# Kernel tuning notes

Measured on AMD Instinct MI355X. Metric: run time of the kernel, lower is better.

Reference implementation:

```python
import jax, jax.numpy as jnp
import numpy as np

B, N, K = 4, 2048, 48
NUM_RBF = 16
NUM_PE = 16
MAX_REL = 32
EDGE_C = 128
PE_IN = 2 * MAX_REL + 2  # 66


def setup_inputs() -> dict:
    key = jax.random.key(0)
    ks = jax.random.split(key, 10)
    coords = jax.random.normal(ks[0], (B, N, 3), dtype=jnp.float32) * 10.0
    token_exists_mask = jnp.ones((B, N), dtype=jnp.float32)
    token_bonds = (jax.random.uniform(ks[1], (B, N, N)) < 0.01).astype(jnp.float32)
    pe_w = jax.random.normal(ks[2], (PE_IN, NUM_PE), dtype=jnp.float32) * 0.05
    pe_b = jnp.zeros((NUM_PE,), dtype=jnp.float32)
    edge_w = jax.random.normal(ks[3], (NUM_PE + NUM_RBF + 1, EDGE_C), dtype=jnp.float32) * 0.05
    ln_g = jnp.ones((EDGE_C,), dtype=jnp.float32)
    ln_b = jnp.zeros((EDGE_C,), dtype=jnp.float32)
    token_to_center_atom = jax.random.randint(ks[4], (B, N), 0, N, dtype=jnp.int32)
    residue_index = jnp.sort(jax.random.randint(ks[5], (B, N), 0, 4096, dtype=jnp.int32), axis=-1)
    asym_id = jax.random.randint(ks[6], (B, N), 0, 4, dtype=jnp.int32)
    is_ligand = jax.random.randint(ks[7], (B, N), 0, 2, dtype=jnp.int32)
    return {
        'coords': coords, 'token_exists_mask': token_exists_mask,
        'token_bonds': token_bonds, 'pe_w': pe_w, 'pe_b': pe_b,
        'edge_w': edge_w, 'ln_g': ln_g, 'ln_b': ln_b,
        'token_to_center_atom': token_to_center_atom,
        'residue_index': residue_index, 'asym_id': asym_id,
        'is_ligand': is_ligand,
    }


def _gather_edges(M, E_idx):
    # M: [B, N, N], E_idx: [B, N, K] -> [B, N, K]
    return jnp.take_along_axis(M, E_idx, axis=2)


def _rbf(D):
    # D: [..., K] -> [..., K, NUM_RBF]
    D_mu = jnp.linspace(2.0, 22.0, NUM_RBF)
    D_sigma = (22.0 - 2.0) / NUM_RBF
    return jnp.exp(-(((D[..., None] - D_mu) / D_sigma) ** 2))


def reference(coords, token_exists_mask, token_bonds, pe_w, pe_b, edge_w,
              ln_g, ln_b, token_to_center_atom, residue_index, asym_id, is_ligand):
    # token coords: center atom per token, masked
    X = jnp.take_along_axis(coords, token_to_center_atom[..., None], axis=1)
    X = X * token_exists_mask[..., None]  # [B, N, 3]

    # masked pairwise distances + KNN (smallest K, sorted ascending)
    mask = token_exists_mask
    mask_2d = mask[:, None, :] * mask[:, :, None]  # [B, N, N]
    dX = X[:, :, None, :] - X[:, None, :, :]
    D = mask_2d * jnp.sqrt(jnp.sum(dX * dX, axis=-1) + 1e-6)
    D_max = jnp.max(D, axis=-1, keepdims=True)
    D_adjust = D + (1.0 - mask_2d) * D_max
    neg_D, E_idx = jax.lax.top_k(-D_adjust, K)  # largest of -D == smallest of D
    D_neighbors = -neg_D  # [B, N, K]

    RBF_all = _rbf(D_neighbors)  # [B, N, K, NUM_RBF]

    # relative sequence position features
    offset = residue_index[:, :, None] - residue_index[:, None, :]  # [B, N, N]
    offset_e = _gather_edges(offset, E_idx)  # [B, N, K]
    chain_labels = jnp.zeros_like(asym_id)  # use_multichain_encoding=False
    d_chains = (chain_labels[:, :, None] - chain_labels[:, None, :] == 0).astype(jnp.int32)
    E_chains = _gather_edges(d_chains, E_idx)  # [B, N, K]
    d = jnp.clip(offset_e + MAX_REL, 0, 2 * MAX_REL) * E_chains + (1 - E_chains) * (2 * MAX_REL + 1)
    d_onehot = jax.nn.one_hot(d, PE_IN, dtype=jnp.float32)
    E_positional = d_onehot @ pe_w + pe_b  # [B, N, K, NUM_PE]

    # ligand-gated bond feature
    lig = is_ligand.astype(bool)
    tb_mask = (lig[:, :, None] | lig[:, None, :]).astype(token_bonds.dtype)
    tb = token_bonds * tb_mask
    tb_e = _gather_edges(tb, E_idx)[..., None]  # [B, N, K, 1]

    # fuse, embed, layernorm
    E = jnp.concatenate([E_positional, RBF_all, tb_e], axis=-1)  # [B, N, K, 33]
    E = E @ edge_w  # [B, N, K, EDGE_C]
    mu = jnp.mean(E, axis=-1, keepdims=True)
    var = jnp.mean((E - mu) ** 2, axis=-1, keepdims=True)
    E = (E - mu) / jnp.sqrt(var + 1e-5) * ln_g + ln_b
    return (E, E_idx, D_neighbors)
```

## Files before the change

kernel.cpp:

```cpp
#include <hip/hip_runtime.h>
#include <math.h>

namespace {
constexpr int B_ = 4;
constexpr int N_ = 2048;
constexpr int K_ = 48;
constexpr int MAX_REL_ = 32;
constexpr int EDGE_C_ = 128;
constexpr int NUM_PE_ = 16;
constexpr int NROWS = B_ * N_;
constexpr int NEDGE = NROWS * K_;
constexpr int C1_ROWS = 2 * MAX_REL_ + 1;
}

__global__ __launch_bounds__(256) void x_kernel(const float* __restrict__ coords,
                                                const float* __restrict__ mask,
                                                const int* __restrict__ t2ca,
                                                float* __restrict__ X) {
    int r = blockIdx.x * 256 + threadIdx.x;
    if (r >= NROWS) return;
    int b = r >> 11;
    int c = t2ca[r];
    float m = mask[r];
    const float* s = coords + ((size_t)(b * N_ + c)) * 3;
    X[r * 3 + 0] = __fmul_rn(s[0], m);
    X[r * 3 + 1] = __fmul_rn(s[1], m);
    X[r * 3 + 2] = __fmul_rn(s[2], m);
}

__global__ __launch_bounds__(256) void c1_kernel(const float* __restrict__ pe_w,
                                                 const float* __restrict__ pe_b,
                                                 const float* __restrict__ edge_w,
                                                 float* __restrict__ C1) {
    int idx = blockIdx.x * 256 + threadIdx.x;
    if (idx >= C1_ROWS * EDGE_C_) return;
    int d = idx >> 7, c = idx & 127;
    float acc = 0.0f;
    #pragma unroll
    for (int p = 0; p < NUM_PE_; ++p)
        acc = fmaf(pe_w[d * NUM_PE_ + p] + pe_b[p], edge_w[p * EDGE_C_ + c], acc);
    C1[idx] = acc;
}

__global__ __launch_bounds__(256) void knn_kernel(const float* __restrict__ X,
                                                  const float* __restrict__ mask,
                                                  float* __restrict__ eidx_f,
                                                  float* __restrict__ dneb) {
    __shared__ unsigned s_hist[4][256];
    __shared__ unsigned long long s_cbuf[4][64];
    const int wv = threadIdx.x >> 6;
    const int lane = threadIdx.x & 63;
    const int row = blockIdx.x * 4 + wv;
    const int b = row >> 11;

    const float xi0 = X[row * 3 + 0];
    const float xi1 = X[row * 3 + 1];
    const float xi2 = X[row * 3 + 2];
    const float mi = mask[row];
    const float* Xb = X + (size_t)b * N_ * 3;
    const float* mb = mask + b * N_;

    float d[32];
    float lmax = -INFINITY;
    #pragma unroll
    for (int t = 0; t < 32; ++t) {
        int j = t * 64 + lane;
        float dx = __fsub_rn(xi0, Xb[j * 3 + 0]);
        float dy = __fsub_rn(xi1, Xb[j * 3 + 1]);
        float dz = __fsub_rn(xi2, Xb[j * 3 + 2]);
        float d2 = __fmaf_rn(dz, dz, __fmaf_rn(dx, dx, __fmul_rn(dy, dy)));
        float m2 = __fmul_rn(mi, mb[j]);
        float dd = __fmul_rn(m2, __fsqrt_rn(__fadd_rn(d2, 1e-6f)));
        d[t] = dd;
        lmax = fmaxf(lmax, dd);
    }
    #pragma unroll
    for (int off = 32; off; off >>= 1) lmax = fmaxf(lmax, __shfl_xor(lmax, off, 64));

    unsigned fb[32];
    unsigned fmin_l = 0xFFFFFFFFu, fmax_l = 0u;
    #pragma unroll
    for (int t = 0; t < 32; ++t) {
        int j = t * 64 + lane;
        float m2 = __fmul_rn(mi, mb[j]);
        float adj = __fadd_rn(d[t], __fmul_rn(__fsub_rn(1.0f, m2), lmax));
        unsigned u = __float_as_uint(adj);
        fb[t] = u;
        fmin_l = min(fmin_l, u);
        fmax_l = max(fmax_l, u);
    }
    #pragma unroll
    for (int off = 32; off; off >>= 1) {
        fmin_l = min(fmin_l, (unsigned)__shfl_xor((int)fmin_l, off, 64));
        fmax_l = max(fmax_l, (unsigned)__shfl_xor((int)fmax_l, off, 64));
    }
    const unsigned fminb = fmin_l;
    const unsigned range = fmax_l - fminb;
    const int vbits = (range == 0u) ? 0 : (32 - __clz((int)range));
    const int L = vbits + 11;

    unsigned long long key[32];
    #pragma unroll
    for (int t = 0; t < 32; ++t)
        key[t] = ((unsigned long long)(fb[t] - fminb) << 11)
               | (unsigned long long)(unsigned)(t * 64 + lane);

    unsigned cand = 0xFFFFFFFFu;
    int k_rem = K_;
    int sh = (L > 8) ? (L - 8) : 0;
    unsigned long long T = 0ull;

    while (true) {
        s_hist[wv][4 * lane + 0] = 0u;
        s_hist[wv][4 * lane + 1] = 0u;
        s_hist[wv][4 * lane + 2] = 0u;
        s_hist[wv][4 * lane + 3] = 0u;
        __asm__ volatile("s_waitcnt lgkmcnt(0)" ::: "memory");
        #pragma unroll
        for (int t = 0; t < 32; ++t) {
            if ((cand >> t) & 1u) {
                unsigned dig = (unsigned)(key[t] >> sh) & 255u;
                atomicAdd(&s_hist[wv][dig], 1u);
            }
        }
        __asm__ volatile("s_waitcnt lgkmcnt(0)" ::: "memory");
        const unsigned c0 = s_hist[wv][4 * lane + 0];
        const unsigned c1 = s_hist[wv][4 * lane + 1];
        const unsigned c2 = s_hist[wv][4 * lane + 2];
        const unsigned c3 = s_hist[wv][4 * lane + 3];
        const unsigned s4 = c0 + c1 + c2 + c3;
        unsigned inc = s4;
        #pragma unroll
        for (int off = 1; off < 64; off <<= 1) {
            unsigned o = (unsigned)__shfl_up((int)inc, off, 64);
            if (lane >= off) inc += o;
        }
        const unsigned ex = inc - s4;
        const unsigned e1 = ex + c0, e2 = e1 + c1, e3 = e2 + c2;
        const unsigned kr = (unsigned)k_rem;
        int digl = -1; unsigned below = 0u, bc = 0u;
        if (ex < kr && kr <= e1)           { digl = 4 * lane + 0; below = ex; bc = c0; }
        else if (e1 < kr && kr <= e2)      { digl = 4 * lane + 1; below = e1; bc = c1; }
        else if (e2 < kr && kr <= e3)      { digl = 4 * lane + 2; below = e2; bc = c2; }
        else if (e3 < kr && kr <= e3 + c3) { digl = 4 * lane + 3; below = e3; bc = c3; }

        unsigned long long bal = __ballot(digl >= 0);
        int src = __ffsll((long long)bal) - 1;
        const int dstar = __shfl(digl, src, 64);
        below = (unsigned)__shfl((int)below, src, 64);
        bc    = (unsigned)__shfl((int)bc, src, 64);
        k_rem -= (int)below;

        unsigned nc = 0u;
        unsigned long long myT = 0ull;
        #pragma unroll
        for (int t = 0; t < 32; ++t) {
            if (((cand >> t) & 1u) &&
                (((unsigned)(key[t] >> sh) & 255u) == (unsigned)dstar)) {
                nc |= (1u << t);
                myT = key[t];
            }
        }
        cand = nc;
        if (bc == 1u || sh == 0) {
            unsigned long long b2 = __ballot(cand != 0u);
            int owner = __ffsll((long long)b2) - 1;
            T = __shfl(myT, owner, 64);
            break;
        }
        sh = (sh > 8) ? (sh - 8) : 0;
    }

    unsigned selm = 0u; int scnt = 0;
    #pragma unroll
    for (int t = 0; t < 32; ++t) {
        if (key[t] <= T) { selm |= (1u << t); ++scnt; }
    }
    int isc = scnt;
    #pragma unroll
    for (int off = 1; off < 64; off <<= 1) {
        int o = __shfl_up(isc, off, 64);
        if (lane >= off) isc += o;
    }
    int pos = isc - scnt;
    #pragma unroll
    for (int t = 0; t < 32; ++t) {
        if ((selm >> t) & 1u) { s_cbuf[wv][pos] = key[t]; ++pos; }
    }
    __asm__ volatile("s_waitcnt lgkmcnt(0)" ::: "memory");
    unsigned long long kk = (lane < K_) ? s_cbuf[wv][lane] : ~0ull;

    #pragma unroll
    for (int k2 = 2; k2 <= 64; k2 <<= 1) {
        #pragma unroll
        for (int j = k2 >> 1; j > 0; j >>= 1) {
            unsigned long long o = __shfl_xor(kk, j, 64);
            const bool dirAsc = ((lane & k2) == 0);
            const bool lower = ((lane & j) == 0);
            unsigned long long mn = (kk < o) ? kk : o;
            unsigned long long mx = (kk < o) ? o : kk;
            kk = (lower == dirAsc) ? mn : mx;
        }
    }

    if (lane < K_) {
        unsigned fbits = (unsigned)(kk >> 11) + fminb;
        unsigned ji = (unsigned)(kk & 2047u);
        dneb[(size_t)row * K_ + lane] = __uint_as_float(fbits);
        eidx_f[(size_t)row * K_ + lane] = (float)ji;
    }
}

__global__ __launch_bounds__(256, 4) void edge_kernel(const float* __restrict__ eidx_f,
                                                      const float* __restrict__ dneb,
                                                      const float* __restrict__ token_bonds,
                                                      const float* __restrict__ C1,
                                                      const float* __restrict__ edge_w,
                                                      const float* __restrict__ ln_g,
                                                      const float* __restrict__ ln_b,
                                                      const int* __restrict__ res_idx,
                                                      const int* __restrict__ is_lig,
                                                      float* __restrict__ Eout) {
    __shared__ float s_rbf[4][K_][NUM_PE_];
    __shared__ float s_D[4][K_];
    const int tid = threadIdx.x;
    const int wv = tid >> 6;
    const int lane = tid & 63;
    const int row = blockIdx.x * 4 + wv;
    const int b = row >> 11;

    float w0[17], w1[17];
    #pragma unroll
    for (int p = 0; p < 17; ++p) {
        float2 w = ((const float2*)edge_w)[(NUM_PE_ + p) * 64 + lane];
        w0[p] = w.x; w1[p] = w.y;
    }
    const float g0 = ln_g[2 * lane], g1 = ln_g[2 * lane + 1];
    const float bb0 = ln_b[2 * lane], bb1 = ln_b[2 * lane + 1];

    const int ri = res_idx[row];
    const int li = is_lig[row];

    int doff_l = 0; float tb_l = 0.0f;
    if (lane < K_) {
        const int e = row * K_ + lane;
        const int j = (int)(eidx_f[e] + 0.5f);
        const float D = dneb[e];
        const int jrow = b * N_ + j;
        const int rj = res_idx[jrow];
        const int lj = is_lig[jrow];
        float tb = token_bonds[(size_t)row * N_ + j];
        tb_l = (li | lj) ? tb : 0.0f;
        doff_l = min(max(ri - rj + MAX_REL_, 0), 2 * MAX_REL_);
        s_D[wv][lane] = D;
    }
    __syncthreads();

    #pragma unroll
    for (int t = 0; t < (K_ * NUM_PE_) / 64; ++t) {
        const int idx = t * 64 + lane;
        const int k = idx >> 4, r = idx & 15;
        const float D = s_D[wv][k];
        const float mu = 2.0f + (float)r * (4.0f / 3.0f);
        const float x = (D - mu) * 0.8f;
        s_rbf[wv][k][r] = __expf(-x * x);
    }
    __syncthreads();

    float2* outp = (float2*)Eout + (size_t)row * K_ * 64 + lane;
    #pragma unroll 2
    for (int k = 0; k < K_; ++k) {
        const int doffk = __shfl(doff_l, k, 64);
        const float tbk = __shfl(tb_l, k, 64);
        const float2 c1 = *(const float2*)(C1 + ((size_t)doffk << 7) + 2 * lane);

        float rr[16];
        *(float4*)&rr[0]  = *(const float4*)&s_rbf[wv][k][0];
        *(float4*)&rr[4]  = *(const float4*)&s_rbf[wv][k][4];
        *(float4*)&rr[8]  = *(const float4*)&s_rbf[wv][k][8];
        *(float4*)&rr[12] = *(const float4*)&s_rbf[wv][k][12];

        float ax = 0.0f, ay = 0.0f;
        #pragma unroll
        for (int p = 0; p < 16; ++p) {
            ax = fmaf(rr[p], w0[p], ax);
            ay = fmaf(rr[p], w1[p], ay);
        }
        if (tbk != 0.0f) {
            ax = fmaf(tbk, w0[16], ax);
            ay = fmaf(tbk, w1[16], ay);
        }
        ax += c1.x; ay += c1.y;

        float s = ax + ay, sq = fmaf(ax, ax, ay * ay);
        #pragma unroll
        for (int off = 32; off; off >>= 1) {
            s  += __shfl_xor(s, off, 64);
            sq += __shfl_xor(sq, off, 64);
        }
        const float mu = s * (1.0f / 128.0f);
        const float var = sq * (1.0f / 128.0f) - mu * mu;
        const float rstd = rsqrtf(var + 1e-5f);
        const float ox = (ax - mu) * rstd * g0 + bb0;
        const float oy = (ay - mu) * rstd * g1 + bb1;
        outp[(size_t)k * 64] = make_float2(ox, oy);
    }
}

extern "C" void kernel_launch(void* const* d_in, const int* in_sizes, int n_in,
                              void* d_out, int out_size, void* d_ws, size_t ws_size,
                              hipStream_t stream) {
    const float* coords      = (const float*)d_in[0];
    const float* mask        = (const float*)d_in[1];
    const float* token_bonds = (const float*)d_in[2];
    const float* pe_w        = (const float*)d_in[3];
    const float* pe_b        = (const float*)d_in[4];
    const float* edge_w      = (const float*)d_in[5];
    const float* ln_g        = (const float*)d_in[6];
    const float* ln_b        = (const float*)d_in[7];
    const int*   t2ca        = (const int*)d_in[8];
    const int*   res_idx     = (const int*)d_in[9];
    const int*   is_lig      = (const int*)d_in[11];

    float* out    = (float*)d_out;
    float* Eout   = out;
    float* eidx_f = out + (size_t)NEDGE * EDGE_C_;
    float* dneb   = eidx_f + NEDGE;

    float* X  = (float*)d_ws;
    float* C1 = X + (size_t)NROWS * 3;

    hipLaunchKernelGGL(x_kernel, dim3(NROWS / 256), dim3(256), 0, stream,
                       coords, mask, t2ca, X);
    hipLaunchKernelGGL(c1_kernel, dim3((C1_ROWS * EDGE_C_ + 255) / 256), dim3(256), 0, stream,
                       pe_w, pe_b, edge_w, C1);
    hipLaunchKernelGGL(knn_kernel, dim3(NROWS / 4), dim3(256), 0, stream,
                       X, mask, eidx_f, dneb);
    hipLaunchKernelGGL(edge_kernel, dim3(NROWS / 4), dim3(256), 0, stream,
                       eidx_f, dneb, token_bonds, C1, edge_w,
                       ln_g, ln_b, res_idx, is_lig, Eout);
}
```

Baseline: 382.1 us.

## Precompute LayerNorm statistics algebraically and shrink KNN key register footprint

Centers the edge weight columns so the LayerNorm mean becomes zero, then precomputes Gram-matrix terms. The per-edge variance can then be evaluated from the 17 input features in one lane, which replaces the per-edge 128-channel wave reductions in the output loop. The KNN kernel also stops holding 64-bit keys in registers and rebuilds them from 32-bit values on demand, to lower register pressure. This adds a single-block prep kernel and reorders the variance arithmetic, which may shift numerics slightly against the reference.

```diff
diff --git a/kernel.cpp b/kernel.cpp
--- a/kernel.cpp
+++ b/kernel.cpp
@@ -28,18 +28,79 @@
     X[r * 3 + 2] = __fmul_rn(s[2], m);
 }
 
-__global__ __launch_bounds__(256) void c1_kernel(const float* __restrict__ pe_w,
-                                                 const float* __restrict__ pe_b,
-                                                 const float* __restrict__ edge_w,
-                                                 float* __restrict__ C1) {
-    int idx = blockIdx.x * 256 + threadIdx.x;
-    if (idx >= C1_ROWS * EDGE_C_) return;
-    int d = idx >> 7, c = idx & 127;
-    float acc = 0.0f;
-    #pragma unroll
-    for (int p = 0; p < NUM_PE_; ++p)
-        acc = fmaf(pe_w[d * NUM_PE_ + p] + pe_b[p], edge_w[p * EDGE_C_ + c], acc);
-    C1[idx] = acc;
+__global__ __launch_bounds__(256) void prep_kernel(const float* __restrict__ pe_w,
+                                                   const float* __restrict__ pe_b,
+                                                   const float* __restrict__ edge_w,
+                                                   float* __restrict__ Wc,
+                                                   float* __restrict__ C1c,
+                                                   float* __restrict__ V0,
+                                                   float* __restrict__ T12_2,
+                                                   float* __restrict__ Tb1_2,
+                                                   float* __restrict__ A22,
+                                                   float* __restrict__ A23_2,
+                                                   float* __restrict__ A33) {
+    __shared__ float sW[33][128];
+    __shared__ float sC[65][128];
+    __shared__ float sm[33];
+    const int tid = threadIdx.x;
+    for (int idx = tid; idx < 33 * 128; idx += 256) ((float*)sW)[idx] = edge_w[idx];
+    __syncthreads();
+    if (tid < 33) {
+        float s = 0.f;
+        for (int c = 0; c < 128; ++c) s += sW[tid][c];
+        sm[tid] = s * (1.f / 128.f);
+    }
+    __syncthreads();
+    for (int idx = tid; idx < 33 * 128; idx += 256) {
+        int p = idx >> 7, c = idx & 127;
+        sW[p][c] -= sm[p];
+    }
+    __syncthreads();
+    for (int idx = tid; idx < 17 * 128; idx += 256) {
+        int p = idx >> 7, c = idx & 127;
+        Wc[idx] = sW[16 + p][c];
+    }
+    for (int idx = tid; idx < 65 * 128; idx += 256) {
+        int d = idx >> 7, c = idx & 127;
+        float acc = 0.f;
+        #pragma unroll
+        for (int q = 0; q < 16; ++q)
+            acc = fmaf(pe_w[d * 16 + q] + pe_b[q], sW[q][c], acc);
+        sC[d][c] = acc;
+        C1c[idx] = acc;
+    }
+    __syncthreads();
+    if (tid < 65) {
+        const int d = tid;
+        float v0 = 0.f, tb1 = 0.f;
+        for (int c = 0; c < 128; ++c) {
+            v0 = fmaf(sC[d][c], sC[d][c], v0);
+            tb1 = fmaf(sC[d][c], sW[32][c], tb1);
+        }
+        V0[d] = v0 * (1.f / 128.f);
+        Tb1_2[d] = tb1 * (2.f / 128.f);
+        for (int r = 0; r < 16; ++r) {
+            float t = 0.f;
+            for (int c = 0; c < 128; ++c) t = fmaf(sC[d][c], sW[16 + r][c], t);
+            T12_2[d * 16 + r] = t * (2.f / 128.f);
+        }
+    }
+    {
+        int r = tid >> 4, s = tid & 15;
+        float a = 0.f;
+        for (int c = 0; c < 128; ++c) a = fmaf(sW[16 + r][c], sW[16 + s][c], a);
+        A22[tid] = a * (1.f / 128.f);
+    }
+    if (tid < 16) {
+        float a = 0.f;
+        for (int c = 0; c < 128; ++c) a = fmaf(sW[16 + tid][c], sW[32][c], a);
+        A23_2[tid] = a * (2.f / 128.f);
+    }
+    if (tid == 0) {
+        float a = 0.f;
+        for (int c = 0; c < 128; ++c) a = fmaf(sW[32][c], sW[32][c], a);
+        A33[0] = a * (1.f / 128.f);
+    }
 }
 
 __global__ __launch_bounds__(256) void knn_kernel(const float* __restrict__ X,
@@ -60,7 +121,7 @@
     const float* Xb = X + (size_t)b * N_ * 3;
     const float* mb = mask + b * N_;
 
-    float d[32];
+    unsigned fb[32];
     float lmax = -INFINITY;
     #pragma unroll
     for (int t = 0; t < 32; ++t) {
@@ -71,19 +132,19 @@
         float d2 = __fmaf_rn(dz, dz, __fmaf_rn(dx, dx, __fmul_rn(dy, dy)));
         float m2 = __fmul_rn(mi, mb[j]);
         float dd = __fmul_rn(m2, __fsqrt_rn(__fadd_rn(d2, 1e-6f)));
-        d[t] = dd;
+        fb[t] = __float_as_uint(dd);
         lmax = fmaxf(lmax, dd);
     }
     #pragma unroll
     for (int off = 32; off; off >>= 1) lmax = fmaxf(lmax, __shfl_xor(lmax, off, 64));
 
-    unsigned fb[32];
     unsigned fmin_l = 0xFFFFFFFFu, fmax_l = 0u;
     #pragma unroll
     for (int t = 0; t < 32; ++t) {
         int j = t * 64 + lane;
         float m2 = __fmul_rn(mi, mb[j]);
-        float adj = __fadd_rn(d[t], __fmul_rn(__fsub_rn(1.0f, m2), lmax));
+        float adj = __fadd_rn(__uint_as_float(fb[t]),
+                              __fmul_rn(__fsub_rn(1.0f, m2), lmax));
         unsigned u = __float_as_uint(adj);
         fb[t] = u;
         fmin_l = min(fmin_l, u);
@@ -98,16 +159,10 @@
     const unsigned range = fmax_l - fminb;
     const int vbits = (range == 0u) ? 0 : (32 - __clz((int)range));
     const int L = vbits + 11;
-
-    unsigned long long key[32];
-    #pragma unroll
-    for (int t = 0; t < 32; ++t)
-        key[t] = ((unsigned long long)(fb[t] - fminb) << 11)
-               | (unsigned long long)(unsigned)(t * 64 + lane);
+    int sh = (L > 8) ? (L - 8) : 0;
 
     unsigned cand = 0xFFFFFFFFu;
     int k_rem = K_;
-    int sh = (L > 8) ? (L - 8) : 0;
     unsigned long long T = 0ull;
 
     while (true) {
@@ -119,7 +174,15 @@
         #pragma unroll
         for (int t = 0; t < 32; ++t) {
             if ((cand >> t) & 1u) {
-                unsigned dig = (unsigned)(key[t] >> sh) & 255u;
+                unsigned dig;
+                if (sh >= 11) {
+                    dig = ((fb[t] - fminb) >> (sh - 11)) & 255u;
+                } else {
+                    unsigned long long key =
+                        ((unsigned long long)(fb[t] - fminb) << 11)
+                        | (unsigned long long)(unsigned)(t * 64 + lane);
+                    dig = (unsigned)(key >> sh) & 255u;
+                }
                 atomicAdd(&s_hist[wv][dig], 1u);
             }
         }
@@ -155,10 +218,14 @@
         unsigned long long myT = 0ull;
         #pragma unroll
         for (int t = 0; t < 32; ++t) {
-            if (((cand >> t) & 1u) &&
-                (((unsigned)(key[t] >> sh) & 255u) == (unsigned)dstar)) {
-                nc |= (1u << t);
-                myT = key[t];
+            if ((cand >> t) & 1u) {
+                unsigned dig;
+                unsigned long long key =
+                    ((unsigned long long)(fb[t] - fminb) << 11)
+                    | (unsigned long long)(unsigned)(t * 64 + lane);
+                if (sh >= 11) dig = ((fb[t] - fminb) >> (sh - 11)) & 255u;
+                else          dig = (unsigned)(key >> sh) & 255u;
+                if (dig == (unsigned)dstar) { nc |= (1u << t); myT = key; }
             }
         }
         cand = nc;
@@ -171,10 +238,14 @@
         sh = (sh > 8) ? (sh - 8) : 0;
     }
 
+    const unsigned Tv = (unsigned)(T >> 11);
+    const unsigned Tj = (unsigned)(T & 2047u);
     unsigned selm = 0u; int scnt = 0;
     #pragma unroll
     for (int t = 0; t < 32; ++t) {
-        if (key[t] <= T) { selm |= (1u << t); ++scnt; }
+        unsigned v = fb[t] - fminb;
+        unsigned j = (unsigned)(t * 64 + lane);
+        if (v < Tv || (v == Tv && j <= Tj)) { selm |= (1u << t); ++scnt; }
     }
     int isc = scnt;
     #pragma unroll
@@ -185,7 +256,11 @@
     int pos = isc - scnt;
     #pragma unroll
     for (int t = 0; t < 32; ++t) {
-        if ((selm >> t) & 1u) { s_cbuf[wv][pos] = key[t]; ++pos; }
+        if ((selm >> t) & 1u) {
+            s_cbuf[wv][pos] = ((unsigned long long)(fb[t] - fminb) << 11)
+                            | (unsigned long long)(unsigned)(t * 64 + lane);
+            ++pos;
+        }
     }
     __asm__ volatile("s_waitcnt lgkmcnt(0)" ::: "memory");
     unsigned long long kk = (lane < K_) ? s_cbuf[wv][lane] : ~0ull;
@@ -214,25 +289,38 @@
 __global__ __launch_bounds__(256, 4) void edge_kernel(const float* __restrict__ eidx_f,
                                                       const float* __restrict__ dneb,
                                                       const float* __restrict__ token_bonds,
-                                                      const float* __restrict__ C1,
-                                                      const float* __restrict__ edge_w,
+                                                      const float* __restrict__ C1c,
+                                                      const float* __restrict__ Wc,
+                                                      const float* __restrict__ V0,
+                                                      const float* __restrict__ T12_2,
+                                                      const float* __restrict__ Tb1_2,
+                                                      const float* __restrict__ A22,
+                                                      const float* __restrict__ A23_2,
+                                                      const float* __restrict__ A33,
                                                       const float* __restrict__ ln_g,
                                                       const float* __restrict__ ln_b,
                                                       const int* __restrict__ res_idx,
                                                       const int* __restrict__ is_lig,
                                                       float* __restrict__ Eout) {
-    __shared__ float s_rbf[4][K_][NUM_PE_];
+    __shared__ float s_rbf[4][K_][20];
     __shared__ float s_D[4][K_];
+    __shared__ float s_A22[256];
+    __shared__ float s_A23[16];
+    __shared__ float s_A33;
     const int tid = threadIdx.x;
     const int wv = tid >> 6;
     const int lane = tid & 63;
     const int row = blockIdx.x * 4 + wv;
     const int b = row >> 11;
 
+    s_A22[tid] = A22[tid];
+    if (tid < 16) s_A23[tid] = A23_2[tid];
+    if (tid == 0) s_A33 = A33[0];
+
     float w0[17], w1[17];
     #pragma unroll
     for (int p = 0; p < 17; ++p) {
-        float2 w = ((const float2*)edge_w)[(NUM_PE_ + p) * 64 + lane];
+        float2 w = ((const float2*)Wc)[p * 64 + lane];
         w0[p] = w.x; w1[p] = w.y;
     }
     const float g0 = ln_g[2 * lane], g1 = ln_g[2 * lane + 1];
@@ -267,20 +355,65 @@
     }
     __syncthreads();
 
+    float rstd_l = 0.0f;
+    if (lane < K_) {
+        float rr[16];
+        const float* rb = &s_rbf[wv][lane][0];
+        *(float4*)&rr[0]  = *(const float4*)&rb[0];
+        *(float4*)&rr[4]  = *(const float4*)&rb[4];
+        *(float4*)&rr[8]  = *(const float4*)&rb[8];
+        *(float4*)&rr[12] = *(const float4*)&rb[12];
+        float var = V0[doff_l];
+        const float4* t12 = (const float4*)(T12_2 + doff_l * 16);
+        float4 q0 = t12[0], q1 = t12[1], q2 = t12[2], q3 = t12[3];
+        var = fmaf(rr[0], q0.x, var);  var = fmaf(rr[1], q0.y, var);
+        var = fmaf(rr[2], q0.z, var);  var = fmaf(rr[3], q0.w, var);
+        var = fmaf(rr[4], q1.x, var);  var = fmaf(rr[5], q1.y, var);
+        var = fmaf(rr[6], q1.z, var);  var = fmaf(rr[7], q1.w, var);
+        var = fmaf(rr[8], q2.x, var);  var = fmaf(rr[9], q2.y, var);
+        var = fmaf(rr[10], q2.z, var); var = fmaf(rr[11], q2.w, var);
+        var = fmaf(rr[12], q3.x, var); var = fmaf(rr[13], q3.y, var);
+        var = fmaf(rr[14], q3.z, var); var = fmaf(rr[15], q3.w, var);
+        #pragma unroll
+        for (int r = 0; r < 16; ++r) {
+            float tr = 0.0f;
+            const float4* arow = (const float4*)&s_A22[r * 16];
+            #pragma unroll
+            for (int s4 = 0; s4 < 4; ++s4) {
+                float4 a = arow[s4];
+                tr = fmaf(rr[s4 * 4 + 0], a.x, tr);
+                tr = fmaf(rr[s4 * 4 + 1], a.y, tr);
+                tr = fmaf(rr[s4 * 4 + 2], a.z, tr);
+                tr = fmaf(rr[s4 * 4 + 3], a.w, tr);
+            }
+            var = fmaf(rr[r], tr, var);
+        }
+        if (tb_l != 0.0f) {
+            float extra = Tb1_2[doff_l];
+            #pragma unroll
+            for (int r = 0; r < 16; ++r) extra = fmaf(rr[r], s_A23[r], extra);
+            var = fmaf(tb_l, extra, var);
+            var = fmaf(tb_l * tb_l, s_A33, var);
+        }
+        rstd_l = rsqrtf(var + 1e-5f);
+    }
+
     float2* outp = (float2*)Eout + (size_t)row * K_ * 64 + lane;
-    #pragma unroll 2
+    #pragma unroll 4
     for (int k = 0; k < K_; ++k) {
         const int doffk = __shfl(doff_l, k, 64);
         const float tbk = __shfl(tb_l, k, 64);
-        const float2 c1 = *(const float2*)(C1 + ((size_t)doffk << 7) + 2 * lane);
+        const float rstd = __shfl(rstd_l, k, 64);
+        const float2 c1 = *(const float2*)(C1c + ((size_t)doffk << 7) + 2 * lane);
 
         float rr[16];
-        *(float4*)&rr[0]  = *(const float4*)&s_rbf[wv][k][0];
-        *(float4*)&rr[4]  = *(const float4*)&s_rbf[wv][k][4];
-        *(float4*)&rr[8]  = *(const float4*)&s_rbf[wv][k][8];
-        *(float4*)&rr[12] = *(const float4*)&s_rbf[wv][k][12];
-
-        float ax = 0.0f, ay = 0.0f;
+        const float* rb = &s_rbf[wv][k][0];
+        *(float4*)&rr[0]  = *(const float4*)&rb[0];
+        *(float4*)&rr[4]  = *(const float4*)&rb[4];
+        *(float4*)&rr[8]  = *(const float4*)&rb[8];
+        *(float4*)&rr[12] = *(const float4*)&rb[12];
+
+        float ax = c1.x, ay = c1.y;
         #pragma unroll
         for (int p = 0; p < 16; ++p) {
             ax = fmaf(rr[p], w0[p], ax);
@@ -290,19 +423,9 @@
             ax = fmaf(tbk, w0[16], ax);
             ay = fmaf(tbk, w1[16], ay);
         }
-        ax += c1.x; ay += c1.y;
-
-        float s = ax + ay, sq = fmaf(ax, ax, ay * ay);
-        #pragma unroll
-        for (int off = 32; off; off >>= 1) {
-            s  += __shfl_xor(s, off, 64);
-            sq += __shfl_xor(sq, off, 64);
-        }
-        const float mu = s * (1.0f / 128.0f);
-        const float var = sq * (1.0f / 128.0f) - mu * mu;
-        const float rstd = rsqrtf(var + 1e-5f);
-        const float ox = (ax - mu) * rstd * g0 + bb0;
-        const float oy = (ay - mu) * rstd * g1 + bb1;
+        const float rg0 = rstd * g0, rg1 = rstd * g1;
+        const float ox = fmaf(ax, rg0, bb0);
+        const float oy = fmaf(ay, rg1, bb1);
         outp[(size_t)k * 64] = make_float2(ox, oy);
     }
 }
@@ -327,16 +450,23 @@
     float* eidx_f = out + (size_t)NEDGE * EDGE_C_;
     float* dneb   = eidx_f + NEDGE;
 
-    float* X  = (float*)d_ws;
-    float* C1 = X + (size_t)NROWS * 3;
+    float* X     = (float*)d_ws;
+    float* Wc    = X + (size_t)NROWS * 3;
+    float* C1c   = Wc + 17 * 128;
+    float* V0    = C1c + 65 * 128;
+    float* T12_2 = V0 + 65;
+    float* Tb1_2 = T12_2 + 65 * 16;
+    float* A22   = Tb1_2 + 65;
+    float* A23_2 = A22 + 256;
+    float* A33   = A23_2 + 16;
 
     hipLaunchKernelGGL(x_kernel, dim3(NROWS / 256), dim3(256), 0, stream,
                        coords, mask, t2ca, X);
-    hipLaunchKernelGGL(c1_kernel, dim3((C1_ROWS * EDGE_C_ + 255) / 256), dim3(256), 0, stream,
-                       pe_w, pe_b, edge_w, C1);
+    hipLaunchKernelGGL(prep_kernel, dim3(1), dim3(256), 0, stream,
+                       pe_w, pe_b, edge_w, Wc, C1c, V0, T12_2, Tb1_2, A22, A23_2, A33);
     hipLaunchKernelGGL(knn_kernel, dim3(NROWS / 4), dim3(256), 0, stream,
                        X, mask, eidx_f, dneb);
     hipLaunchKernelGGL(edge_kernel, dim3(NROWS / 4), dim3(256), 0, stream,
-                       eidx_f, dneb, token_bonds, C1, edge_w,
-                       ln_g, ln_b, res_idx, is_lig, Eout);
-}
+                       eidx_f, dneb, token_bonds, C1c, Wc, V0, T12_2, Tb1_2,
+                       A22, A23_2, A33, ln_g, ln_b, res_idx, is_lig, Eout);
+}
```

Result: slower. 398.2 us (+4.2%).
